# Kernel tuning notes

Hardware: AMD Instinct MI355X
Metric: run time of the kernel (lower is better)

## Reference

```python
import jax, jax.numpy as jnp
import numpy as np

# Orbital structure for basis {A: [2s, 2p, 1d]} -> full_basis l values
LS = [0, 0, 1, 1, 2]
DIMS = [2 * l + 1 for l in LS]            # [1,1,3,3,5]
OFFS = np.concatenate([[0], np.cumsum(DIMS)]).astype(int)
NORB = int(sum(DIMS))                      # 13

# Upper-triangular orbital-pair layout of the flat feature vector
PAIRS = []
_off = 0
for _i in range(len(LS)):
    for _j in range(_i, len(LS)):
        PAIRS.append((_i, _j, _off))
        _off += DIMS[_i] * DIMS[_j]
FEAT_DIM = _off                            # 107

N_ATOMS, N_EDGES, N_KPTS = 256, 4096, 4


def _assemble_blocks(feat):
    """[B, FEAT_DIM] -> [B, NORB, NORB], upper-tri orbital blocks, 0.5 on diagonal pairs."""
    B = feat.shape[0]
    blk = jnp.zeros((B, NORB, NORB), feat.dtype)
    for (i, j, o) in PAIRS:
        di, dj = DIMS[i], DIMS[j]
        f = 0.5 if i == j else 1.0
        blk = blk.at[:, OFFS[i]:OFFS[i] + di, OFFS[j]:OFFS[j] + dj].set(
            f * feat[:, o:o + di * dj].reshape(B, di, dj))
    return blk


def setup_inputs() -> dict:
    key = jax.random.key(0)
    k1, k2, k3, k4, k5 = jax.random.split(key, 5)
    return {
        "orbpair_hopping": jax.random.normal(k1, (N_EDGES, FEAT_DIM), jnp.float32),
        "orbpair_onsite": jax.random.normal(k2, (N_ATOMS, FEAT_DIM), jnp.float32),
        "kpoints": jax.random.uniform(k3, (N_KPTS, 3), jnp.float32),
        "edge_cell_shift": jax.random.randint(k4, (N_EDGES, 3), -3, 4).astype(jnp.float32),
        "edge_index": jax.random.randint(k5, (2, N_EDGES), 0, N_ATOMS),
    }


def reference(orbpair_hopping, orbpair_onsite, kpoints, edge_cell_shift, edge_index):
    hop = _assemble_blocks(orbpair_hopping)      # [E, norb, norb]
    onsite = _assemble_blocks(orbpair_onsite)    # [N, norb, norb]
    N, K = onsite.shape[0], kpoints.shape[0]
    cplx = jnp.complex64

    # phase[k, e] = exp(-i 2pi k . R_e)
    phase = jnp.exp(-2j * jnp.pi * (kpoints @ edge_cell_shift.T)).astype(cplx)  # [K, E]

    # H(k) in block form [K, N, N, norb, norb]
    blk = jnp.zeros((K, N, N, NORB, NORB), cplx)
    ar = jnp.arange(N)
    blk = blk.at[:, ar, ar].set(onsite.astype(cplx)[None])  # diagonal onsite blocks
    ei, ej = edge_index[0], edge_index[1]
    blk = blk.at[:, ei, ej].add(phase[:, :, None, None] * hop.astype(cplx)[None])

    H = blk.transpose(0, 1, 3, 2, 4).reshape(K, N * NORB, N * NORB)
    return H + jnp.conj(jnp.swapaxes(H, 1, 2))  # hermitianize
```

## Files before the change

### kernel.cpp

```cpp
#include <hip/hip_runtime.h>

#define NORB 13
#define FEAT 107
#define TWO_PI 6.28318530717958647692f

__device__ __forceinline__ void map_pq(int p, int q, int& idx, float& scl) {
    const int DIMS[5] = {1, 1, 3, 3, 5};
    const int OFFS[5] = {0, 1, 2, 5, 8};
    idx = -1; scl = 0.0f;
    int o = 0;
    #pragma unroll
    for (int i = 0; i < 5; ++i) {
        #pragma unroll
        for (int j = i; j < 5; ++j) {
            int di = DIMS[i], dj = DIMS[j];
            if (p >= OFFS[i] && p < OFFS[i] + di && q >= OFFS[j] && q < OFFS[j] + dj) {
                idx = o + (p - OFFS[i]) * dj + (q - OFFS[j]);
                scl = (i == j) ? 0.5f : 1.0f;
            }
            o += di * dj;
        }
    }
}

__global__ void zero_kernel(float4* __restrict__ out, long n4) {
    long i = (long)blockIdx.x * blockDim.x + threadIdx.x;
    long stride = (long)gridDim.x * blockDim.x;
    float4 z = make_float4(0.f, 0.f, 0.f, 0.f);
    for (; i < n4; i += stride) out[i] = z;
}

template <int CPX>
__global__ void onsite_kernel(const float* __restrict__ onsite, float* __restrict__ out,
                              int K, long nn) {
    int a = blockIdx.x;
    int t = threadIdx.x;
    if (t >= NORB * NORB) return;
    int p = t / NORB, q = t % NORB;
    int i1, i2; float s1, s2;
    map_pq(p, q, i1, s1);
    map_pq(q, p, i2, s2);
    const float* f = onsite + (long)a * FEAT;
    float v = 0.0f;
    if (i1 >= 0) v += s1 * f[i1];
    if (i2 >= 0) v += s2 * f[i2];
    long row = (long)a * NORB + p;
    long col = (long)a * NORB + q;
    for (int k = 0; k < K; ++k) {
        long off = (((long)k * nn + row) * nn + col) * CPX;
        out[off] = v;
    }
}

template <int CPX>
__global__ void edge_kernel(const float* __restrict__ hop, const float* __restrict__ kpts,
                            const float* __restrict__ shift, const int* __restrict__ eidx,
                            float* __restrict__ out, int E, int K, long nn) {
    int e = blockIdx.x;
    int t = threadIdx.x;
    __shared__ float phc[16], phs[16];
    int ei = eidx[e];
    int ej = eidx[E + e];
    if (t < K && t < 16) {
        float rx = shift[(long)e * 3 + 0];
        float ry = shift[(long)e * 3 + 1];
        float rz = shift[(long)e * 3 + 2];
        float th = -TWO_PI * (kpts[t * 3 + 0] * rx + kpts[t * 3 + 1] * ry + kpts[t * 3 + 2] * rz);
        float s, c;
        __sincosf(th, &s, &c);
        phc[t] = c; phs[t] = s;
    }
    __syncthreads();
    if (t >= NORB * NORB) return;
    int p = t / NORB, q = t % NORB;
    int idx; float scl;
    map_pq(p, q, idx, scl);
    if (idx < 0) return;
    float v = scl * hop[(long)e * FEAT + idx];
    long r1 = (long)ei * NORB + p, c1 = (long)ej * NORB + q;
    long r2 = (long)ej * NORB + q, c2 = (long)ei * NORB + p;
    for (int k = 0; k < K; ++k) {
        float pr = phc[k], pi = phs[k];
        long o1 = (((long)k * nn + r1) * nn + c1) * CPX;
        long o2 = (((long)k * nn + r2) * nn + c2) * CPX;
        atomicAdd(&out[o1], pr * v);
        atomicAdd(&out[o2], pr * v);
        if (CPX == 2) {
            atomicAdd(&out[o1 + 1], pi * v);
            atomicAdd(&out[o2 + 1], -pi * v);
        }
    }
}

extern "C" void kernel_launch(void* const* d_in, const int* in_sizes, int n_in,
                              void* d_out, int out_size, void* d_ws, size_t ws_size,
                              hipStream_t stream) {
    const float* hop  = (const float*)d_in[0];
    const float* ons  = (const float*)d_in[1];
    const float* kpt  = (const float*)d_in[2];
    const float* shf  = (const float*)d_in[3];
    const int*   eidx = (const int*)d_in[4];

    int E = in_sizes[0] / FEAT;
    int N = in_sizes[1] / FEAT;
    int K = in_sizes[2] / 3;
    long nn = (long)N * NORB;

    float* out = (float*)d_out;

    long knn2 = (long)K * nn * nn * 2;
    int cpx = ((long)out_size >= knn2) ? 2 : 1;

    long n4 = (long)out_size / 4;
    zero_kernel<<<2048, 256, 0, stream>>>((float4*)out, n4);

    if (cpx == 2) {
        onsite_kernel<2><<<N, 192, 0, stream>>>(ons, out, K, nn);
        edge_kernel<2><<<E, 192, 0, stream>>>(hop, kpt, shf, eidx, out, E, K, nn);
    } else {
        onsite_kernel<1><<<N, 192, 0, stream>>>(ons, out, K, nn);
        edge_kernel<1><<<E, 192, 0, stream>>>(hop, kpt, shf, eidx, out, E, K, nn);
    }
}
```

Before: 79.71 us.

## Replace atomic scatter with per-block-pair linked-list gather and gated zeroing

Builds per (atom a, atom b) linked lists of directed edges in workspace and precomputes phases. One block per occupied pair then sums its contributions in registers and writes each output element once, with no atomics. The zero fill skips float4s that the paint pass will fully overwrite. The fast path is specialized to N=256 and K=4, and it adds extra launches plus a per-element head lookup in the zero pass.

```diff
diff --git a/kernel.cpp b/kernel.cpp
--- a/kernel.cpp
+++ b/kernel.cpp
@@ -3,6 +3,8 @@
 #define NORB 13
 #define FEAT 107
 #define TWO_PI 6.28318530717958647692f
+#define NN 3328
+#define NN2 (NN * NN)
 
 __device__ __forceinline__ void map_pq(int p, int q, int& idx, float& scl) {
     const int DIMS[5] = {1, 1, 3, 3, 5};
@@ -22,6 +24,113 @@
         }
     }
 }
+
+
+__global__ void init_kernel(int4* __restrict__ head4, int* __restrict__ pairlist,
+                            int* __restrict__ counter) {
+    int t = blockIdx.x * blockDim.x + threadIdx.x;
+    head4[t] = make_int4(-1, -1, -1, -1);
+    if (t < 256) pairlist[t] = t * 257;
+    if (t == 0) *counter = 256;
+}
+
+__global__ void fill_kernel(const int* __restrict__ eidx, const float* __restrict__ kpt,
+                            const float* __restrict__ shf,
+                            int* __restrict__ head, int* __restrict__ nxt,
+                            int* __restrict__ pairlist, int* __restrict__ counter,
+                            float* __restrict__ phases, int E, int K) {
+    int tid = blockIdx.x * blockDim.x + threadIdx.x;
+    if (tid >= 2 * E) return;
+    int e = tid >> 1, dir = tid & 1;
+    int ei = eidx[e], ej = eidx[E + e];
+    int a = dir ? ej : ei;
+    int b = dir ? ei : ej;
+    int pid = a * 256 + b;
+    int old = atomicExch(&head[pid], tid);
+    nxt[tid] = old;
+    if (old < 0 && a != b) {
+        int pos = atomicAdd(counter, 1);
+        pairlist[pos] = pid;
+    }
+    if (dir == 0) {
+        float rx = shf[e * 3 + 0], ry = shf[e * 3 + 1], rz = shf[e * 3 + 2];
+        for (int k = 0; k < K; ++k) {
+            float th = -TWO_PI * (kpt[k * 3] * rx + kpt[k * 3 + 1] * ry + kpt[k * 3 + 2] * rz);
+            float s, c;
+            __sincosf(th, &s, &c);
+            phases[(e * K + k) * 2]     = c;
+            phases[(e * K + k) * 2 + 1] = s;
+        }
+    }
+}
+
+__global__ void zero_gated_kernel(float4* __restrict__ out4, const int* __restrict__ head,
+                                  long n4) {
+    long i = (long)blockIdx.x * blockDim.x + threadIdx.x;
+    long stride = (long)gridDim.x * blockDim.x;
+    float4 z = make_float4(0.f, 0.f, 0.f, 0.f);
+    for (; i < n4; i += stride) {
+        unsigned ci  = (unsigned)(i * 2);
+        unsigned rem = ci % NN2;
+        unsigned row = rem / NN;
+        unsigned c   = rem - row * NN;
+        unsigned a   = row / 13u;
+        unsigned b0  = c / 13u;
+        unsigned b1  = (c + 1u) / 13u;
+        bool p0 = (a == b0) || head[a * 256u + b0] >= 0;
+        bool p1 = (b1 == b0) ? p0 : ((a == b1) || head[a * 256u + b1] >= 0);
+        if (!(p0 && p1)) out4[i] = z;
+    }
+}
+
+__global__ void paint_kernel(const float* __restrict__ hop, const float* __restrict__ ons,
+                             const int* __restrict__ head, const int* __restrict__ nxt,
+                             const int* __restrict__ pairlist, const int* __restrict__ counter,
+                             const float* __restrict__ phases, float* __restrict__ out,
+                             int K) {
+    int w = blockIdx.x;
+    if (w >= *counter) return;
+    int t = threadIdx.x;
+    if (t >= NORB * NORB) return;
+    int pid = pairlist[w];
+    int a = pid >> 8, b = pid & 255;
+    int p = t / NORB, q = t - p * NORB;
+    int i0, i1; float s0, s1;
+    map_pq(p, q, i0, s0);
+    map_pq(q, p, i1, s1);
+    float ar[4] = {0.f, 0.f, 0.f, 0.f}, ai[4] = {0.f, 0.f, 0.f, 0.f};
+    if (a == b) {
+        const float* f = ons + (long)a * FEAT;
+        float v = 0.f;
+        if (i0 >= 0) v += s0 * f[i0];
+        if (i1 >= 0) v += s1 * f[i1];
+        #pragma unroll
+        for (int k = 0; k < 4; ++k) ar[k] += v;
+    }
+    for (int it = head[pid]; it >= 0; it = nxt[it]) {
+        int e = it >> 1, dir = it & 1;
+        float hv;
+        if (dir == 0) hv = (i0 >= 0) ? s0 * hop[(long)e * FEAT + i0] : 0.f;
+        else          hv = (i1 >= 0) ? s1 * hop[(long)e * FEAT + i1] : 0.f;
+        const float* ph = phases + (long)e * K * 2;
+        if (dir == 0) {
+            #pragma unroll
+            for (int k = 0; k < 4; ++k) { ar[k] += ph[2 * k] * hv; ai[k] += ph[2 * k + 1] * hv; }
+        } else {
+            #pragma unroll
+            for (int k = 0; k < 4; ++k) { ar[k] += ph[2 * k] * hv; ai[k] -= ph[2 * k + 1] * hv; }
+        }
+    }
+    long row = (long)a * NORB + p;
+    long col = (long)b * NORB + q;
+    #pragma unroll
+    for (int k = 0; k < 4; ++k) {
+        long off = (((long)k * NN + row) * NN + col) * 2;
+        out[off]     = ar[k];
+        out[off + 1] = ai[k];
+    }
+}
+
 
 __global__ void zero_kernel(float4* __restrict__ out, long n4) {
     long i = (long)blockIdx.x * blockDim.x + threadIdx.x;
@@ -92,6 +201,7 @@
     }
 }
 
+
 extern "C" void kernel_launch(void* const* d_in, const int* in_sizes, int n_in,
                               void* d_out, int out_size, void* d_ws, size_t ws_size,
                               hipStream_t stream) {
@@ -107,18 +217,44 @@
     long nn = (long)N * NORB;
 
     float* out = (float*)d_out;
-
     long knn2 = (long)K * nn * nn * 2;
-    int cpx = ((long)out_size >= knn2) ? 2 : 1;
-
-    long n4 = (long)out_size / 4;
-    zero_kernel<<<2048, 256, 0, stream>>>((float4*)out, n4);
-
-    if (cpx == 2) {
-        onsite_kernel<2><<<N, 192, 0, stream>>>(ons, out, K, nn);
-        edge_kernel<2><<<E, 192, 0, stream>>>(hop, kpt, shf, eidx, out, E, K, nn);
+
+    size_t off_head  = 0;
+    size_t off_next  = off_head + 65536 * sizeof(int);
+    size_t off_plist = off_next + (size_t)2 * E * sizeof(int);
+    size_t off_cnt   = off_plist + (size_t)(256 + 2 * E) * sizeof(int);
+    size_t off_phase = (off_cnt + 4 + 127) & ~(size_t)127;
+    size_t ws_need   = off_phase + (size_t)E * K * 2 * sizeof(float);
+
+    bool fast = (N == 256) && (K == 4) && (nn == NN) &&
+                ((long)out_size == knn2) && (ws_size >= ws_need);
+
+    if (fast) {
+        char* ws = (char*)d_ws;
+        int*   head   = (int*)(ws + off_head);
+        int*   nxt    = (int*)(ws + off_next);
+        int*   plist  = (int*)(ws + off_plist);
+        int*   cnt    = (int*)(ws + off_cnt);
+        float* phases = (float*)(ws + off_phase);
+
+        init_kernel<<<64, 256, 0, stream>>>((int4*)head, plist, cnt);
+        int fill_blocks = (2 * E + 255) / 256;
+        fill_kernel<<<fill_blocks, 256, 0, stream>>>(eidx, kpt, shf, head, nxt,
+                                                     plist, cnt, phases, E, K);
+        long n4 = (long)out_size / 4;
+        zero_gated_kernel<<<2048, 256, 0, stream>>>((float4*)out, head, n4);
+        paint_kernel<<<256 + 2 * E, 192, 0, stream>>>(hop, ons, head, nxt, plist,
+                                                      cnt, phases, out, K);
     } else {
-        onsite_kernel<1><<<N, 192, 0, stream>>>(ons, out, K, nn);
-        edge_kernel<1><<<E, 192, 0, stream>>>(hop, kpt, shf, eidx, out, E, K, nn);
-    }
-}
+        int cpx = ((long)out_size >= knn2) ? 2 : 1;
+        long n4 = (long)out_size / 4;
+        zero_kernel<<<2048, 256, 0, stream>>>((float4*)out, n4);
+        if (cpx == 2) {
+            onsite_kernel<2><<<N, 192, 0, stream>>>(ons, out, K, nn);
+            edge_kernel<2><<<E, 192, 0, stream>>>(hop, kpt, shf, eidx, out, E, K, nn);
+        } else {
+            onsite_kernel<1><<<N, 192, 0, stream>>>(ons, out, K, nn);
+            edge_kernel<1><<<E, 192, 0, stream>>>(hop, kpt, shf, eidx, out, E, K, nn);
+        }
+    }
+}
```

Measured after the change: 80.97 us. No clear change (+1.6%).

## Bucket edges per atom and build each block-row in shared memory without atomics

Applied to the files above, without the earlier changes.

Adds a preprocessing pass that bins edges by source atom (both directions) into per-atom lists and precomputes per-edge phases. A fused kernel then assigns one block per (k-point, atom, half block-row), accumulates the onsite and hopping contributions into shared-memory tiles, and writes each output row once, with nontemporal zero stores for empty blocks. This replaces the separate global zero pass and the scattered global atomics with one streaming write. A fallback path that uses atomics covers atoms with too many neighbours. The fast path is specialised to N=256, K=4 and is limited by fixed capacities.

```diff
diff --git a/kernel.cpp b/kernel.cpp
--- a/kernel.cpp
+++ b/kernel.cpp
@@ -3,6 +3,21 @@
 #define NORB 13
 #define FEAT 107
 #define TWO_PI 6.28318530717958647692f
+#define NN 3328
+#define ROWF (NN * 2)
+#define R4 (NN / 2)
+#define EMAX 4096
+#define CAP 128
+#define MAXS 64
+
+typedef float f4 __attribute__((ext_vector_type(4)));
+
+__device__ int   g_acnt[256];
+__device__ int   g_items[256 * CAP];
+__device__ int   g_ovh[256];
+__device__ int   g_ovnxt[2 * EMAX];
+__device__ int   g_ovitem[2 * EMAX];
+__device__ float g_phases[EMAX * 8];
 
 __device__ __forceinline__ void map_pq(int p, int q, int& idx, float& scl) {
     const int DIMS[5] = {1, 1, 3, 3, 5};
@@ -23,11 +38,222 @@
     }
 }
 
+
+__global__ void init_kernel() {
+    int t = threadIdx.x;
+    g_acnt[t] = 0;
+    g_ovh[t] = -1;
+}
+
+__global__ void fill_kernel(const int* __restrict__ eidx, const float* __restrict__ kpt,
+                            const float* __restrict__ shf, int E, int K) {
+    int tid = blockIdx.x * blockDim.x + threadIdx.x;
+    if (tid >= 2 * E) return;
+    int e = tid >> 1, dir = tid & 1;
+    int ei = eidx[e], ej = eidx[E + e];
+    int a = dir ? ej : ei;
+    int b = dir ? ei : ej;
+    int pk = (b << 13) | (e << 1) | dir;
+    int slot = atomicAdd(&g_acnt[a], 1);
+    if (slot < CAP) {
+        g_items[a * CAP + slot] = pk;
+    } else {
+        int old = atomicExch(&g_ovh[a], tid);
+        g_ovnxt[tid] = old;
+        g_ovitem[tid] = pk;
+    }
+    if (dir == 0) {
+        float rx = shf[e * 3 + 0], ry = shf[e * 3 + 1], rz = shf[e * 3 + 2];
+        for (int k = 0; k < K; ++k) {
+            float th = -TWO_PI * (kpt[k * 3] * rx + kpt[k * 3 + 1] * ry + kpt[k * 3 + 2] * rz);
+            float s, c;
+            __sincosf(th, &s, &c);
+            g_phases[e * 8 + k * 2]     = c;
+            g_phases[e * 8 + k * 2 + 1] = s;
+        }
+    }
+}
+
+__global__ __launch_bounds__(256)
+void fused3_kernel(const float* __restrict__ hop, const float* __restrict__ ons,
+                   float* __restrict__ out) {
+    int z = blockIdx.x;
+    int k = z >> 9;
+    int a = (z >> 1) & 255;
+    int half = z & 1;
+    int rbase = half ? 7 : 0;
+    int nrows = half ? 6 : 7;
+    int t = threadIdx.x;
+
+    __shared__ int ilist[CAP];
+    __shared__ unsigned char present[256];
+    __shared__ unsigned char smap[256];
+    __shared__ unsigned char sblk[MAXS];
+    __shared__ unsigned long long wmask[4];
+    __shared__ float2 pblk[MAXS][91];
+
+    int n = g_acnt[a];
+    present[t] = 0;
+    __syncthreads();
+    int nb = n < CAP ? n : CAP;
+    for (int i = t; i < nb; i += 256) {
+        int pk = g_items[a * CAP + i];
+        ilist[i] = pk;
+        present[(pk >> 13) & 255] = 1;
+    }
+    if (t == 0) present[a] = 1;
+    __syncthreads();
+
+    unsigned long long m = __ballot(present[t] != 0);
+    int w = t >> 6;
+    if ((t & 63) == 0) wmask[w] = m;
+    __syncthreads();
+    int nslots = __popcll(wmask[0]) + __popcll(wmask[1]) +
+                 __popcll(wmask[2]) + __popcll(wmask[3]);
+    bool fallback = (n > CAP) || (nslots > MAXS);
+
+    if (!fallback) {
+        if (present[t]) {
+            int pre = 0;
+            #pragma unroll
+            for (int i = 0; i < 4; ++i) if (i < w) pre += __popcll(wmask[i]);
+            pre += __popcll(wmask[w] & ((1ull << (t & 63)) - 1ull));
+            smap[t] = (unsigned char)pre;
+            sblk[pre] = (unsigned char)t;
+        } else {
+            smap[t] = 255;
+        }
+        __syncthreads();
+
+        float2* pf = &pblk[0][0];
+        for (int i = t; i < nslots * 91; i += 256) pf[i] = make_float2(0.f, 0.f);
+        __syncthreads();
+
+        if (t < 91) {
+            int p = rbase + t / 13, q = t % 13;
+            int i0, i1; float s0, s1;
+            map_pq(p, q, i0, s0);
+            map_pq(q, p, i1, s1);
+            {
+                const float* f = ons + (long)a * FEAT;
+                float v = 0.f;
+                if (i0 >= 0) v += s0 * f[i0];
+                if (i1 >= 0) v += s1 * f[i1];
+                pblk[smap[a]][t].x += v;
+            }
+            for (int i = 0; i < nb; ++i) {
+                int pk = ilist[i];
+                int b = (pk >> 13) & 255;
+                int e = (pk >> 1) & 4095;
+                int dir = pk & 1;
+                int s = smap[b];
+                float hv = dir ? ((i1 >= 0) ? s1 * hop[(long)e * FEAT + i1] : 0.f)
+                               : ((i0 >= 0) ? s0 * hop[(long)e * FEAT + i0] : 0.f);
+                float pr = g_phases[e * 8 + k * 2];
+                float pi = g_phases[e * 8 + k * 2 + 1];
+                float2 v = pblk[s][t];
+                v.x += pr * hv;
+                v.y += (dir ? -pi : pi) * hv;
+                pblk[s][t] = v;
+            }
+        }
+        __syncthreads();
+
+        float4* out4 = (float4*)out;
+        int ntask8 = nslots * nrows * 8;
+        for (int it0 = t; it0 < ntask8; it0 += 256) {
+            int lane = it0 & 7;
+            int task = it0 >> 3;
+            int s = task % nslots;
+            int rr = task / nslots;
+            int b = sblk[s];
+            int fb = (13 * b) >> 1;
+            int fe = (13 * b + 12) >> 1;
+            int f = fb + lane;
+            if (f > fe) continue;
+            int c0 = 2 * f, c1 = c0 + 1;
+            float4 v;
+            {
+                int bc = (unsigned)c0 / 13u;
+                int mm = smap[bc];
+                if (mm != 255) { float2 pv = pblk[mm][rr * 13 + (c0 - 13 * bc)]; v.x = pv.x; v.y = pv.y; }
+                else           { v.x = 0.f; v.y = 0.f; }
+            }
+            {
+                int bc = (unsigned)c1 / 13u;
+                int mm = smap[bc];
+                if (mm != 255) { float2 pv = pblk[mm][rr * 13 + (c1 - 13 * bc)]; v.z = pv.x; v.w = pv.y; }
+                else           { v.z = 0.f; v.w = 0.f; }
+            }
+            long off4 = (long)(k * NN + a * 13 + rbase + rr) * R4 + f;
+            out4[off4] = v;
+        }
+
+        f4 z4 = {0.f, 0.f, 0.f, 0.f};
+        for (int rr = 0; rr < nrows; ++rr) {
+            long rowb = (long)(k * NN + a * 13 + rbase + rr) * R4;
+            for (int f = t; f < R4; f += 256) {
+                int b0 = (unsigned)(2 * f) / 13u;
+                int b1 = (unsigned)(2 * f + 1) / 13u;
+                if (smap[b0] != 255 || smap[b1] != 255) continue;
+                __builtin_nontemporal_store(z4, (f4*)((float4*)out + rowb + f));
+            }
+        }
+    } else {
+        f4 z4 = {0.f, 0.f, 0.f, 0.f};
+        for (int rr = 0; rr < nrows; ++rr) {
+            long rowb = (long)(k * NN + a * 13 + rbase + rr) * R4;
+            for (int f = t; f < R4; f += 256)
+                __builtin_nontemporal_store(z4, (f4*)((float4*)out + rowb + f));
+        }
+        __syncthreads();
+        int maxt = nrows * 13;
+        if (t < maxt) {
+            int p = rbase + t / 13, q = t % 13;
+            int i0, i1; float s0, s1;
+            map_pq(p, q, i0, s0);
+            map_pq(q, p, i1, s1);
+            {
+                const float* f = ons + (long)a * FEAT;
+                float v = 0.f;
+                if (i0 >= 0) v += s0 * f[i0];
+                if (i1 >= 0) v += s1 * f[i1];
+                long off = (long)(k * NN + a * 13 + p) * ROWF + (a * 13 + q) * 2;
+                atomicAdd(&out[off], v);
+            }
+            int nbl = n < CAP ? n : CAP;
+            for (int i = 0; i < nbl; ++i) {
+                int pk = g_items[a * CAP + i];
+                int b = (pk >> 13) & 255, e = (pk >> 1) & 4095, dir = pk & 1;
+                float hv = dir ? ((i1 >= 0) ? s1 * hop[(long)e * FEAT + i1] : 0.f)
+                               : ((i0 >= 0) ? s0 * hop[(long)e * FEAT + i0] : 0.f);
+                float pr = g_phases[e * 8 + k * 2];
+                float pi = g_phases[e * 8 + k * 2 + 1];
+                long off = (long)(k * NN + a * 13 + p) * ROWF + (b * 13 + q) * 2;
+                atomicAdd(&out[off], pr * hv);
+                atomicAdd(&out[off + 1], (dir ? -pi : pi) * hv);
+            }
+            for (int it = g_ovh[a]; it >= 0; it = g_ovnxt[it]) {
+                int pk = g_ovitem[it];
+                int b = (pk >> 13) & 255, e = (pk >> 1) & 4095, dir = pk & 1;
+                float hv = dir ? ((i1 >= 0) ? s1 * hop[(long)e * FEAT + i1] : 0.f)
+                               : ((i0 >= 0) ? s0 * hop[(long)e * FEAT + i0] : 0.f);
+                float pr = g_phases[e * 8 + k * 2];
+                float pi = g_phases[e * 8 + k * 2 + 1];
+                long off = (long)(k * NN + a * 13 + p) * ROWF + (b * 13 + q) * 2;
+                atomicAdd(&out[off], pr * hv);
+                atomicAdd(&out[off + 1], (dir ? -pi : pi) * hv);
+            }
+        }
+    }
+}
+
+
 __global__ void zero_kernel(float4* __restrict__ out, long n4) {
     long i = (long)blockIdx.x * blockDim.x + threadIdx.x;
     long stride = (long)gridDim.x * blockDim.x;
-    float4 z = make_float4(0.f, 0.f, 0.f, 0.f);
-    for (; i < n4; i += stride) out[i] = z;
+    float4 zz = make_float4(0.f, 0.f, 0.f, 0.f);
+    for (; i < n4; i += stride) out[i] = zz;
 }
 
 template <int CPX>
@@ -92,6 +318,7 @@
     }
 }
 
+
 extern "C" void kernel_launch(void* const* d_in, const int* in_sizes, int n_in,
                               void* d_out, int out_size, void* d_ws, size_t ws_size,
                               hipStream_t stream) {
@@ -107,18 +334,25 @@
     long nn = (long)N * NORB;
 
     float* out = (float*)d_out;
-
     long knn2 = (long)K * nn * nn * 2;
-    int cpx = ((long)out_size >= knn2) ? 2 : 1;
-
-    long n4 = (long)out_size / 4;
-    zero_kernel<<<2048, 256, 0, stream>>>((float4*)out, n4);
-
-    if (cpx == 2) {
-        onsite_kernel<2><<<N, 192, 0, stream>>>(ons, out, K, nn);
-        edge_kernel<2><<<E, 192, 0, stream>>>(hop, kpt, shf, eidx, out, E, K, nn);
+
+    bool fast = (N == 256) && (K == 4) && (E <= EMAX) &&
+                ((long)out_size == knn2);
+
+    if (fast) {
+        init_kernel<<<1, 256, 0, stream>>>();
+        fill_kernel<<<(2 * E + 255) / 256, 256, 0, stream>>>(eidx, kpt, shf, E, K);
+        fused3_kernel<<<2048, 256, 0, stream>>>(hop, ons, out);
     } else {
-        onsite_kernel<1><<<N, 192, 0, stream>>>(ons, out, K, nn);
-        edge_kernel<1><<<E, 192, 0, stream>>>(hop, kpt, shf, eidx, out, E, K, nn);
-    }
-}
+        int cpx = ((long)out_size >= knn2) ? 2 : 1;
+        long n4 = (long)out_size / 4;
+        zero_kernel<<<2048, 256, 0, stream>>>((float4*)out, n4);
+        if (cpx == 2) {
+            onsite_kernel<2><<<N, 192, 0, stream>>>(ons, out, K, nn);
+            edge_kernel<2><<<E, 192, 0, stream>>>(hop, kpt, shf, eidx, out, E, K, nn);
+        } else {
+            onsite_kernel<1><<<N, 192, 0, stream>>>(ons, out, K, nn);
+            edge_kernel<1><<<E, 192, 0, stream>>>(hop, kpt, shf, eidx, out, E, K, nn);
+        }
+    }
+}
```

After: 80.76 us. No clear change (+1.3%).
